# Kernel optimization log

Hardware: AMD Instinct MI355X
Metric: run time of the kernel (lower is better)

## Reference

```python
import jax, jax.numpy as jnp
import numpy as np

T, B, F = 197, 64, 768      # tokens (hardcoded 197 in module), batch, width
N, K = 8, 2                 # num_experts, top-k
CAP = int(197 * 1.0 * K / N)  # capacity = 49
H = 4 * F                   # expert hidden (c_fc out)
G = F // 4                  # gate hidden


def setup_inputs() -> dict:
    key = jax.random.key(0)
    ks = jax.random.split(key, 9)
    s = 0.02
    return {
        "x":   jax.random.normal(ks[0], (T, B, F), jnp.float32),
        # gate: Linear(F, F/4) -> ReLU -> Linear(F/4, N)
        "Wg1": jax.random.normal(ks[1], (F, G), jnp.float32) * s,
        "bg1": jnp.zeros((G,), jnp.float32),
        "Wg2": jax.random.normal(ks[2], (G, N), jnp.float32) * s,
        "bg2": jnp.zeros((N,), jnp.float32),
        # experts: per-expert Linear(F, 4F) -> ReLU -> Linear(4F, F), stacked over N
        "W1":  jax.random.normal(ks[3], (N, F, H), jnp.float32) * s,
        "b1":  jnp.zeros((N, H), jnp.float32),
        "W2":  jax.random.normal(ks[4], (N, H, F), jnp.float32) * s,
        "b2":  jnp.zeros((N, F), jnp.float32),
    }


def reference(x, Wg1, bg1, Wg2, bg2, W1, b1, W2, b2):
    # gating: softmax over experts (dim=2)
    logits = jax.nn.relu(x @ Wg1 + bg1) @ Wg2 + bg2          # [T,B,N]
    gw = jax.nn.softmax(logits, axis=2)                      # [T,B,N]

    # dense all-expert MLP (as-written: every expert on every token)
    h = jax.nn.relu(jnp.einsum('tbf,nfh->tbnh', x, W1) + b1)  # [T,B,N,H]
    eo = jnp.einsum('tbnh,nhf->tbnf', h, W2) + b2             # [T,B,N,F]

    # top-k expert mask (dim=2)
    _, idx = jax.lax.top_k(gw, K)                             # [T,B,K]
    mask_exp = jnp.any(jnp.arange(N)[None, None, None, :] == idx[..., None], axis=2)
    cw = gw * mask_exp                                        # [T,B,N]

    # capacity mask: top-CAP tokens per (batch, expert) along dim 0
    cwT = jnp.moveaxis(cw, 0, -1)                             # [B,N,T]
    _, idx2 = jax.lax.top_k(cwT, CAP)                         # [B,N,CAP]
    mask_cap = jnp.any(jnp.arange(T)[None, None, None, :] == idx2[..., None], axis=2)  # [B,N,T]
    fw = cw * jnp.moveaxis(mask_cap, -1, 0)                   # [T,B,N]

    # combine selected expert outputs, residual-style subtract
    out = jnp.einsum('tbnf,tbn->tbf', eo, fw) - x             # [T,B,F]
    return out
```

## Files before the change

kernel.cpp:

```cpp
#include <hip/hip_runtime.h>
#include <hip/hip_bf16.h>
#include <math.h>
#include <stdint.h>

#define T_ 197
#define B_ 64
#define F_ 768
#define N_ 8
#define CAP_ 49
#define H_ 3072
#define G_ 192
#define TB_ (T_*B_)
#define NBN_ (B_*N_)
#define ME_ 3200
#define MR_ 3136
#define MT_ 25600
#define HCF_ 384
#define NPF_ 8

using bf16x8 = __attribute__((ext_vector_type(8))) short;
using f32x4  = __attribute__((ext_vector_type(4))) float;

__device__ __forceinline__ unsigned short f2bf(float v) {
    __hip_bfloat16 h = __float2bfloat16(v);
    return __builtin_bit_cast(unsigned short, h);
}
__device__ __forceinline__ float bf2f(unsigned short u) {
    unsigned int w = ((unsigned int)u) << 16;
    return __builtin_bit_cast(float, w);
}

#define GLL16(g, l) __builtin_amdgcn_global_load_lds( \
    (const __attribute__((address_space(1))) unsigned int*)(uintptr_t)(g), \
    (__attribute__((address_space(3))) unsigned int*)(uintptr_t)(l), 16, 0, 0)

__device__ __forceinline__ int xcd_swz(int bid, int nblk) {
    int q = nblk >> 3, r = nblk & 7;
    int xcd = bid & 7, idx = bid >> 3;
    int base = (xcd < r) ? xcd * (q + 1) : r * (q + 1) + (xcd - r) * q;
    return base + idx;
}

__global__ void k_init_out(const float* __restrict__ x, float* __restrict__ out) {
    int i = blockIdx.x * blockDim.x + threadIdx.x;
    const float4* xv = (const float4*)x;
    float4* ov = (float4*)out;
    float4 v = xv[i];
    ov[i] = make_float4(-v.x, -v.y, -v.z, -v.w);
}

__global__ __launch_bounds__(256) void k_gate1(
        const float* __restrict__ x, const float* __restrict__ Wg1,
        float* __restrict__ gs_part) {
    __shared__ float xs[2][64 * 32];
    __shared__ float wt[2][64][36];
    int bid = blockIdx.x;
    int bm = bid % 197; int rest = bid / 197;
    int bn = rest % 3, kh = rest / 3;
    int m0 = bm * 64, n0 = bn * 64, k0 = kh * 384;
    int tid = threadIdx.x, lane = tid & 63, wid = tid >> 6;
    int tc = tid & 15, tr = tid >> 4;
    float acc[4][4] = {};
    const float* xbase = x + (size_t)m0 * F_ + k0;
    float wreg[8];

    auto issueX = [&](int buf, int t) {
        int kb = t * 32;
        #pragma unroll
        for (int i = 0; i < 2; ++i) {
            int r0 = wid * 16 + i * 8;
            GLL16(xbase + (size_t)(r0 + (lane >> 3)) * F_ + kb + (lane & 7) * 4,
                  &xs[buf][r0 * 32]);
        }
    };
    auto loadW = [&](int t) {
        int kb = k0 + t * 32;
        #pragma unroll
        for (int i = 0; i < 8; ++i) {
            int idx = tid + i * 256;
            int kk = idx >> 6, nn = idx & 63;
            wreg[i] = Wg1[(size_t)(kb + kk) * G_ + n0 + nn];
        }
    };
    auto writeW = [&](int buf) {
        #pragma unroll
        for (int i = 0; i < 8; ++i) {
            int idx = tid + i * 256;
            int kk = idx >> 6, nn = idx & 63;
            wt[buf][nn][kk] = wreg[i];
        }
    };

    loadW(0); issueX(0, 0); writeW(0);
    __syncthreads();
    int cur = 0;
    for (int t = 0; t < 12; ++t) {
        if (t < 11) { loadW(t + 1); issueX(cur ^ 1, t + 1); }
        const float* xc = &xs[cur][0];
        #pragma unroll
        for (int kq = 0; kq < 8; ++kq) {
            float4 a[4], b[4];
            #pragma unroll
            for (int i = 0; i < 4; ++i) a[i] = *(const float4*)(xc + (tr * 4 + i) * 32 + kq * 4);
            #pragma unroll
            for (int j = 0; j < 4; ++j) b[j] = *(const float4*)&wt[cur][tc + 16 * j][kq * 4];
            #pragma unroll
            for (int i = 0; i < 4; ++i)
                #pragma unroll
                for (int j = 0; j < 4; ++j)
                    acc[i][j] += a[i].x * b[j].x + a[i].y * b[j].y + a[i].z * b[j].z + a[i].w * b[j].w;
        }
        if (t < 11) writeW(cur ^ 1);
        __syncthreads();
        cur ^= 1;
    }
    float* gp = gs_part + (size_t)kh * TB_ * G_;
    #pragma unroll
    for (int j = 0; j < 4; ++j) {
        int c = n0 + tc + 16 * j;
        #pragma unroll
        for (int i = 0; i < 4; ++i) {
            int r = m0 + tr * 4 + i;
            gp[(size_t)r * G_ + c] = acc[i][j];
        }
    }
}

__global__ __launch_bounds__(256) void k_gate2(
        const float* __restrict__ gs_part, const float* __restrict__ bg1,
        const float* __restrict__ Wg2, const float* __restrict__ bg2,
        float* __restrict__ cw, int* __restrict__ ecnt) {
    __shared__ float gsh[32][200];
    __shared__ float wg2s[G_ * N_];
    __shared__ float lg[32][8];
    int tid = threadIdx.x;
    int id0 = blockIdx.x * 32;

    for (int i = tid; i < 32 * 48; i += 256) {
        int r = i / 48, c4 = i % 48;
        const float* p0 = gs_part + (size_t)(id0 + r) * G_ + c4 * 4;
        float4 a = *(const float4*)p0;
        float4 b = *(const float4*)(p0 + (size_t)TB_ * G_);
        float4 g = *(const float4*)(bg1 + c4 * 4);
        float4 v;
        v.x = fmaxf(a.x + b.x + g.x, 0.f);
        v.y = fmaxf(a.y + b.y + g.y, 0.f);
        v.z = fmaxf(a.z + b.z + g.z, 0.f);
        v.w = fmaxf(a.w + b.w + g.w, 0.f);
        ((float4*)&gsh[r][0])[c4] = v;
    }
    for (int i = tid; i < G_ * N_; i += 256) wg2s[i] = Wg2[i];
    __syncthreads();

    int tk = tid >> 3, n = tid & 7;
    float a = bg2[n];
    for (int k = 0; k < G_; ++k) a += gsh[tk][k] * wg2s[k * N_ + n];
    lg[tk][n] = a;
    __syncthreads();

    if (tid < 32) {
        int tk2 = tid;
        float p[8];
        float m = lg[tk2][0];
        #pragma unroll
        for (int nn = 1; nn < 8; ++nn) m = fmaxf(m, lg[tk2][nn]);
        float s = 0.f;
        #pragma unroll
        for (int nn = 0; nn < 8; ++nn) { p[nn] = expf(lg[tk2][nn] - m); s += p[nn]; }
        float inv = 1.f / s;
        #pragma unroll
        for (int nn = 0; nn < 8; ++nn) p[nn] *= inv;
        int i1 = 0; float v1 = p[0];
        #pragma unroll
        for (int nn = 1; nn < 8; ++nn) if (p[nn] > v1) { v1 = p[nn]; i1 = nn; }
        int i2 = -1; float v2 = -1.f;
        #pragma unroll
        for (int nn = 0; nn < 8; ++nn) if (nn != i1 && p[nn] > v2) { v2 = p[nn]; i2 = nn; }
        int id = id0 + tk2;
        int t = id / B_, b = id % B_;
        ecnt[id] = 0;
        #pragma unroll
        for (int nn = 0; nn < 8; ++nn) {
            float v = (nn == i1 || nn == i2) ? p[nn] : 0.f;
            cw[((size_t)(b * N_ + nn)) * T_ + t] = v;
        }
    }
}

__global__ __launch_bounds__(256) void k_gate(
        const float* __restrict__ x, const float* __restrict__ Wg1,
        const float* __restrict__ bg1, const float* __restrict__ Wg2,
        const float* __restrict__ bg2, float* __restrict__ cw,
        int* __restrict__ ecnt) {
    __shared__ float xsh[8][F_];
    __shared__ float gsl[8][G_];
    __shared__ float lg[8][N_];
    int tid = threadIdx.x;
    int id0 = blockIdx.x * 8;

    int gid = blockIdx.x * 256 + tid;
    if (gid < TB_ && ecnt) ecnt[gid] = 0;

    const float4* xv = (const float4*)(x + (size_t)id0 * F_);
    float4* xshv = (float4*)&xsh[0][0];
    for (int idx = tid; idx < 8 * (F_/4); idx += 256) xshv[idx] = xv[idx];
    __syncthreads();

    if (tid < G_) {
        float acc[8];
        float bb = bg1[tid];
        #pragma unroll
        for (int tk = 0; tk < 8; ++tk) acc[tk] = bb;
        for (int k = 0; k < F_; ++k) {
            float w = Wg1[k * G_ + tid];
            #pragma unroll
            for (int tk = 0; tk < 8; ++tk) acc[tk] += xsh[tk][k] * w;
        }
        #pragma unroll
        for (int tk = 0; tk < 8; ++tk) gsl[tk][tid] = fmaxf(acc[tk], 0.f);
    }
    __syncthreads();

    if (tid < 64) {
        int tk = tid >> 3, n = tid & 7;
        float acc = bg2[n];
        for (int k = 0; k < G_; ++k) acc += gsl[tk][k] * Wg2[k * N_ + n];
        lg[tk][n] = acc;
    }
    __syncthreads();

    if (tid < 8) {
        int tk = tid;
        float p[8];
        float m = lg[tk][0];
        #pragma unroll
        for (int n = 1; n < 8; ++n) m = fmaxf(m, lg[tk][n]);
        float s = 0.f;
        #pragma unroll
        for (int n = 0; n < 8; ++n) { p[n] = expf(lg[tk][n] - m); s += p[n]; }
        float inv = 1.f / s;
        #pragma unroll
        for (int n = 0; n < 8; ++n) p[n] *= inv;
        int i1 = 0; float v1 = p[0];
        #pragma unroll
        for (int n = 1; n < 8; ++n) if (p[n] > v1) { v1 = p[n]; i1 = n; }
        int i2 = -1; float v2 = -1.f;
        #pragma unroll
        for (int n = 0; n < 8; ++n) if (n != i1 && p[n] > v2) { v2 = p[n]; i2 = n; }
        int id = id0 + tk;
        int t = id / B_, b = id % B_;
        #pragma unroll
        for (int n = 0; n < 8; ++n) {
            float v = (n == i1 || n == i2) ? p[n] : 0.f;
            cw[((size_t)(b * N_ + n)) * T_ + t] = v;
        }
    }
}

__global__ __launch_bounds__(256) void k_capacity(
        const float* __restrict__ cw, int* __restrict__ toks,
        float* __restrict__ wts, int* __restrict__ counts,
        int* __restrict__ ecnt, int* __restrict__ erow) {
    __shared__ float v[T_];
    __shared__ int keep[T_];
    int tid = threadIdx.x;
    int bn = blockIdx.x;
    int b = bn >> 3, n = bn & 7;
    if (tid < T_) v[tid] = cw[(size_t)bn * T_ + tid];
    __syncthreads();
    int kp = 0; float my = 0.f;
    if (tid < T_) {
        my = v[tid];
        int rank = 0;
        for (int t2 = 0; t2 < T_; ++t2) {
            float vt = v[t2];
            rank += (vt > my) || (vt == my && t2 < tid);
        }
        kp = (rank < CAP_) && (my > 0.f);
    }
    if (tid < T_) keep[tid] = kp;
    __syncthreads();
    if (tid < T_ && kp) {
        int slot = 0;
        for (int t2 = 0; t2 < T_; ++t2) slot += (t2 < tid) ? keep[t2] : 0;
        toks[bn * CAP_ + slot] = tid;
        wts[bn * CAP_ + slot] = my;
        if (ecnt) {
            int orow = tid * B_ + b;
            int pos = atomicAdd(&ecnt[orow], 1);
            erow[orow * 2 + pos] = n * ME_ + b * CAP_ + slot;
        }
    }
    if (tid == 0) {
        int tot = 0;
        for (int t2 = 0; t2 < T_; ++t2) tot += keep[t2];
        counts[bn] = tot;
    }
}

__global__ __launch_bounds__(256) void k_repack(
        const float* __restrict__ W, unsigned short* __restrict__ WT, int K, int J) {
    __shared__ float tile[64][65];
    int bid = blockIdx.x;
    int nk = K >> 6, nj = J >> 6;
    int kt = bid % nk; bid /= nk;
    int jt = bid % nj; int e = bid / nj;
    int k0 = kt * 64, j0 = jt * 64;
    int tid = threadIdx.x;
    int jr = (tid & 15) << 2;
    int kr = tid >> 4;
    const float* src = W + ((size_t)e * K + k0) * J + j0;
    #pragma unroll
    for (int i = 0; i < 4; ++i) {
        float4 v = *(const float4*)(src + (size_t)(kr + 16 * i) * J + jr);
        *(float4*)&tile[kr + 16 * i][jr] = v;
    }
    __syncthreads();
    int c = tid & 7;
    int jrow = tid >> 3;
    #pragma unroll
    for (int i = 0; i < 2; ++i) {
        int j = jrow + 32 * i;
        float f[8];
        #pragma unroll
        for (int s = 0; s < 8; ++s) f[s] = tile[c * 8 + s][j];
        uint4 u;
        u.x = f2bf(f[0]) | ((unsigned)f2bf(f[1]) << 16);
        u.y = f2bf(f[2]) | ((unsigned)f2bf(f[3]) << 16);
        u.z = f2bf(f[4]) | ((unsigned)f2bf(f[5]) << 16);
        u.w = f2bf(f[6]) | ((unsigned)f2bf(f[7]) << 16);
        int jg = j0 + j;
        char* drow = (char*)WT + ((size_t)e * J + jg) * (size_t)K * 2 + (size_t)(k0 >> 6) * 128;
        *(uint4*)(drow + ((c << 4) ^ ((jg & 7) << 4))) = u;
    }
}

__global__ __launch_bounds__(256) void k_gather(
        const float* __restrict__ x, const int* __restrict__ toks,
        const int* __restrict__ counts, unsigned short* __restrict__ Xg) {
    int gi = blockIdx.x * 256 + threadIdx.x;
    int R = gi / 96, c = gi - R * 96;
    int e = R / ME_, re = R - e * ME_;
    uint4 val = make_uint4(0u, 0u, 0u, 0u);
    if (re < MR_) {
        int g = re / CAP_, slot = re - g * CAP_;
        int bn = g * N_ + e;
        if (slot < counts[bn]) {
            int t = toks[bn * CAP_ + slot];
            const float* xp = x + ((size_t)t * B_ + g) * F_ + c * 8;
            float4 v0 = *(const float4*)xp;
            float4 v1 = *(const float4*)(xp + 4);
            val.x = f2bf(v0.x) | ((unsigned)f2bf(v0.y) << 16);
            val.y = f2bf(v0.z) | ((unsigned)f2bf(v0.w) << 16);
            val.z = f2bf(v1.x) | ((unsigned)f2bf(v1.y) << 16);
            val.w = f2bf(v1.z) | ((unsigned)f2bf(v1.w) << 16);
        }
    }
    int w = (c * 16) & 127;
    char* dst = (char*)Xg + (size_t)R * 1536 + (c >> 3) * 128 + (w ^ ((R & 7) << 4));
    *(uint4*)dst = val;
}

__global__ __launch_bounds__(256) void k_gemm1(
        const unsigned short* __restrict__ W1T, const unsigned short* __restrict__ Xg,
        const float* __restrict__ b1, unsigned short* __restrict__ Hg,
        int e0, int nblk) {
    __shared__ char ldsA[2][16384];
    __shared__ char ldsB[2][16384];
    int swzb = xcd_swz(blockIdx.x, nblk);
    int mt = swzb / 24;
    int jt = swzb % 24;
    int em = mt / 25;
    int e = e0 + em;
    int tid = threadIdx.x, lane = tid & 63, wid = tid >> 6;
    int lr8 = lane >> 3, sl = (lane & 7) << 4;
    const char* Ab = (const char*)W1T + ((size_t)e * H_ + (size_t)jt * 128) * (F_ * 2);
    const char* Bb = (const char*)Xg + ((size_t)e * ME_ + (size_t)(mt % 25) * 128) * (F_ * 2);
    f32x4 acc[4][4] = {};
    int swz = (lane & 7) << 4;
    int q16 = (lane >> 4) << 4;

    auto stage = [&](int buf, int it) {
        int kb = it << 7;
        #pragma unroll
        for (int i = 0; i < 4; ++i) {
            int lr = wid * 32 + i * 8 + lr8;
            GLL16(Ab + (size_t)lr * 1536 + kb + sl, ldsA[buf] + (wid * 32 + i * 8) * 128);
            GLL16(Bb + (size_t)lr * 1536 + kb + sl, ldsB[buf] + (wid * 32 + i * 8) * 128);
        }
    };

    stage(0, 0);
    __syncthreads();
    int cur = 0;
    for (int it = 0; it < 12; ++it) {
        if (it < 11) stage(cur ^ 1, it + 1);
        const char* la = ldsA[cur] + ((wid & 1) * 64) * 128;
        const char* lb = ldsB[cur] + ((wid >> 1) * 64) * 128;
        #pragma unroll
        for (int ks = 0; ks < 2; ++ks) {
            bf16x8 af[4], bfr[4];
            int kk = (ks * 64 + q16) ^ swz;
            #pragma unroll
            for (int t = 0; t < 4; ++t) {
                int ro = (16 * t + (lane & 15)) * 128;
                af[t]  = *(const bf16x8*)(la + ro + kk);
                bfr[t] = *(const bf16x8*)(lb + ro + kk);
            }
            #pragma unroll
            for (int ti = 0; ti < 4; ++ti)
                #pragma unroll
                for (int tm = 0; tm < 4; ++tm)
                    acc[ti][tm] = __builtin_amdgcn_mfma_f32_16x16x32_bf16(af[ti], bfr[tm], acc[ti][tm], 0, 0, 0);
        }
        __syncthreads();
        cur ^= 1;
    }
    int jl0 = jt * 128 + (wid & 1) * 64;
    int ml0 = mt * 128 + (wid >> 1) * 64;
    const float* b1p = b1 + (size_t)e * H_;
    #pragma unroll
    for (int tj = 0; tj < 4; ++tj) {
        int jc = jl0 + 16 * tj + ((lane >> 4) << 2);
        float bb0 = b1p[jc], bb1 = b1p[jc + 1], bb2 = b1p[jc + 2], bb3 = b1p[jc + 3];
        #pragma unroll
        for (int tm = 0; tm < 4; ++tm) {
            int m = ml0 + 16 * tm + (lane & 15);
            f32x4 a = acc[tj][tm];
            unsigned int u0 = f2bf(fmaxf(a[0] + bb0, 0.f)) | ((unsigned)f2bf(fmaxf(a[1] + bb1, 0.f)) << 16);
            unsigned int u1 = f2bf(fmaxf(a[2] + bb2, 0.f)) | ((unsigned)f2bf(fmaxf(a[3] + bb3, 0.f)) << 16);
            int w = (jc * 2) & 127;
            char* dst = (char*)Hg + (size_t)m * (H_ * 2) + ((jc * 2) & ~127) + (w ^ ((m & 7) << 4));
            *(uint2*)dst = make_uint2(u0, u1);
        }
    }
}

__global__ __launch_bounds__(256) void k_gemm2(
        const unsigned short* __restrict__ W2T, const unsigned short* __restrict__ Hg,
        const float* __restrict__ b2, const float* __restrict__ wts,
        const int* __restrict__ counts, unsigned short* __restrict__ Og,
        int e0, int nblk) {
    __shared__ char ldsA[2][16384];
    __shared__ char ldsB[2][16384];
    int swzb = xcd_swz(blockIdx.x, nblk);
    int mt = swzb / 6;
    int ft = swzb % 6;
    int em = mt / 25;
    int e = e0 + em;
    int tid = threadIdx.x, lane = tid & 63, wid = tid >> 6;
    int lr8 = lane >> 3, sl = (lane & 7) << 4;
    const char* Ab = (const char*)W2T + ((size_t)e * F_ + (size_t)ft * 128) * (H_ * 2);
    const char* Bb = (const char*)Hg + (size_t)mt * 128 * (H_ * 2);
    f32x4 acc[4][4] = {};
    int swz = (lane & 7) << 4;
    int q16 = (lane >> 4) << 4;

    auto stage = [&](int buf, int it) {
        int kb = it << 7;
        #pragma unroll
        for (int i = 0; i < 4; ++i) {
            int lr = wid * 32 + i * 8 + lr8;
            GLL16(Ab + (size_t)lr * 6144 + kb + sl, ldsA[buf] + (wid * 32 + i * 8) * 128);
            GLL16(Bb + (size_t)lr * 6144 + kb + sl, ldsB[buf] + (wid * 32 + i * 8) * 128);
        }
    };

    stage(0, 0);
    __syncthreads();
    int cur = 0;
    for (int it = 0; it < 48; ++it) {
        if (it < 47) stage(cur ^ 1, it + 1);
        const char* la = ldsA[cur] + ((wid & 1) * 64) * 128;
        const char* lb = ldsB[cur] + ((wid >> 1) * 64) * 128;
        #pragma unroll
        for (int ks = 0; ks < 2; ++ks) {
            bf16x8 af[4], bfr[4];
            int kk = (ks * 64 + q16) ^ swz;
            #pragma unroll
            for (int t = 0; t < 4; ++t) {
                int ro = (16 * t + (lane & 15)) * 128;
                af[t]  = *(const bf16x8*)(la + ro + kk);
                bfr[t] = *(const bf16x8*)(lb + ro + kk);
            }
            #pragma unroll
            for (int ti = 0; ti < 4; ++ti)
                #pragma unroll
                for (int tm = 0; tm < 4; ++tm)
                    acc[ti][tm] = __builtin_amdgcn_mfma_f32_16x16x32_bf16(af[ti], bfr[tm], acc[ti][tm], 0, 0, 0);
        }
        __syncthreads();
        cur ^= 1;
    }
    int fl0 = ft * 128 + (wid & 1) * 64;
    int ml0 = mt * 128 + (wid >> 1) * 64;
    const float* b2p = b2 + (size_t)e * F_;
    float fwv[4]; int mrow[4];
    #pragma unroll
    for (int tm = 0; tm < 4; ++tm) {
        int m = ml0 + 16 * tm + (lane & 15);
        int re = m - em * ME_;
        float fw = 0.f;
        if (re < MR_) {
            int g = re / CAP_;
            int slot = re - g * CAP_;
            int bn = g * N_ + e;
            if (slot < counts[bn]) fw = wts[bn * CAP_ + slot];
        }
        fwv[tm] = fw;
        mrow[tm] = e0 * ME_ + m;
    }
    #pragma unroll
    for (int tf = 0; tf < 4; ++tf) {
        int f = fl0 + 16 * tf + ((lane >> 4) << 2);
        float c0 = b2p[f], c1 = b2p[f + 1], c2 = b2p[f + 2], c3 = b2p[f + 3];
        #pragma unroll
        for (int tm = 0; tm < 4; ++tm) {
            f32x4 a = acc[tf][tm];
            float fw = fwv[tm];
            unsigned int u0 = f2bf(fw * (a[0] + c0)) | ((unsigned)f2bf(fw * (a[1] + c1)) << 16);
            unsigned int u1 = f2bf(fw * (a[2] + c2)) | ((unsigned)f2bf(fw * (a[3] + c3)) << 16);
            *(uint2*)((char*)Og + (size_t)mrow[tm] * (F_ * 2) + f * 2) = make_uint2(u0, u1);
        }
    }
}

__global__ __launch_bounds__(256) void k_combine(
        const float* __restrict__ x, const unsigned short* __restrict__ Og,
        const int* __restrict__ ecnt, const int* __restrict__ erow,
        float* __restrict__ out) {
    int idx = blockIdx.x * 256 + threadIdx.x;
    int row = idx / 192, c4 = idx - row * 192;
    float4 s = make_float4(0.f, 0.f, 0.f, 0.f);
    int c = ecnt[row];
    if (c > 0) {
        ushort4 u = *(const ushort4*)(Og + (size_t)erow[row * 2] * F_ + c4 * 4);
        s.x += bf2f(u.x); s.y += bf2f(u.y); s.z += bf2f(u.z); s.w += bf2f(u.w);
    }
    if (c > 1) {
        ushort4 u = *(const ushort4*)(Og + (size_t)erow[row * 2 + 1] * F_ + c4 * 4);
        s.x += bf2f(u.x); s.y += bf2f(u.y); s.z += bf2f(u.z); s.w += bf2f(u.w);
    }
    float4 xv = ((const float4*)x)[idx];
    ((float4*)out)[idx] = make_float4(s.x - xv.x, s.y - xv.y, s.z - xv.z, s.w - xv.w);
}

__global__ __launch_bounds__(HCF_) void k_fc1(
        const float* __restrict__ x, const float* __restrict__ W1,
        const float* __restrict__ b1, const int* __restrict__ toks,
        const int* __restrict__ counts, __hip_bfloat16* __restrict__ h, int pass) {
    __shared__ float xs[25][F_];
    int tid = threadIdx.x;
    int bn = blockIdx.x >> 1;
    int half = blockIdx.x & 1;
    int r0 = half * 25;
    int b = bn >> 3, n = bn & 7;
    int c = counts[bn];
    for (int idx = tid; idx < 25 * (F_/4); idx += HCF_) {
        int r = idx / (F_/4), k4 = idx % (F_/4);
        int gr = r0 + r;
        float4 val = make_float4(0.f, 0.f, 0.f, 0.f);
        if (gr < c) {
            int t = toks[bn * CAP_ + gr];
            val = ((const float4*)(x + ((size_t)(t * B_ + b)) * F_))[k4];
        }
        ((float4*)&xs[r][0])[k4] = val;
    }
    __syncthreads();
    int j = pass * HCF_ + tid;
    const float* w1p = W1 + (size_t)n * F_ * H_ + j;
    float bias = b1[n * H_ + j];
    float acc[25];
    #pragma unroll
    for (int r = 0; r < 25; ++r) acc[r] = bias;
    const float4* xsv = (const float4*)&xs[0][0];
    for (int k4 = 0; k4 < F_/4; ++k4) {
        float w0 = w1p[(size_t)(4*k4+0) * H_];
        float w1v = w1p[(size_t)(4*k4+1) * H_];
        float w2v = w1p[(size_t)(4*k4+2) * H_];
        float w3v = w1p[(size_t)(4*k4+3) * H_];
        #pragma unroll
        for (int r = 0; r < 25; ++r) {
            float4 xv = xsv[r * (F_/4) + k4];
            acc[r] += xv.x*w0 + xv.y*w1v + xv.z*w2v + xv.w*w3v;
        }
    }
    __hip_bfloat16* hp = h + ((size_t)bn * CAP_ + r0) * HCF_ + tid;
    #pragma unroll
    for (int r = 0; r < 25; ++r) {
        int gr = r0 + r;
        if (gr < CAP_) hp[(size_t)r * HCF_] = __float2bfloat16(fmaxf(acc[r], 0.f));
    }
}

__global__ __launch_bounds__(768) void k_fc2(
        const float* __restrict__ W2, const float* __restrict__ b2,
        const int* __restrict__ toks, const float* __restrict__ wts,
        const int* __restrict__ counts, const __hip_bfloat16* __restrict__ h,
        float* __restrict__ out, int pass) {
    __shared__ float hs[CAP_][HCF_];
    int tid = threadIdx.x;
    int bn = blockIdx.x;
    int c = counts[bn];
    if (c == 0) return;
    int b = bn >> 3, n = bn & 7;
    const ushort4* hv = (const ushort4*)(h + (size_t)bn * CAP_ * HCF_);
    for (int idx = tid; idx < CAP_ * (HCF_/4); idx += 768) {
        ushort4 u = hv[idx];
        float4 fv;
        fv.x = __bfloat162float(*(const __hip_bfloat16*)&u.x);
        fv.y = __bfloat162float(*(const __hip_bfloat16*)&u.y);
        fv.z = __bfloat162float(*(const __hip_bfloat16*)&u.z);
        fv.w = __bfloat162float(*(const __hip_bfloat16*)&u.w);
        ((float4*)&hs[0][0])[idx] = fv;
    }
    __syncthreads();
    int f = tid;
    const float* w2p = W2 + (size_t)n * H_ * F_ + (size_t)(pass * HCF_) * F_ + f;
    float acc[CAP_];
    #pragma unroll
    for (int r = 0; r < CAP_; ++r) acc[r] = 0.f;
    for (int j4 = 0; j4 < HCF_/4; ++j4) {
        float w0 = w2p[(size_t)(4*j4+0) * F_];
        float w1v = w2p[(size_t)(4*j4+1) * F_];
        float w2v = w2p[(size_t)(4*j4+2) * F_];
        float w3v = w2p[(size_t)(4*j4+3) * F_];
        #pragma unroll
        for (int r = 0; r < CAP_; ++r) {
            float4 hh = ((const float4*)&hs[r][0])[j4];
            acc[r] += hh.x*w0 + hh.y*w1v + hh.z*w2v + hh.w*w3v;
        }
    }
    float bias = (pass == 0) ? b2[n * F_ + f] : 0.f;
    #pragma unroll
    for (int r = 0; r < CAP_; ++r) {
        if (r < c) {
            int t = toks[bn * CAP_ + r];
            float fw = wts[bn * CAP_ + r];
            atomicAdd(&out[((size_t)(t * B_ + b)) * F_ + f], fw * (acc[r] + bias));
        }
    }
}

extern "C" void kernel_launch(void* const* d_in, const int* in_sizes, int n_in,
                              void* d_out, int out_size, void* d_ws, size_t ws_size,
                              hipStream_t stream) {
    const float* x   = (const float*)d_in[0];
    const float* Wg1 = (const float*)d_in[1];
    const float* bg1 = (const float*)d_in[2];
    const float* Wg2 = (const float*)d_in[3];
    const float* bg2 = (const float*)d_in[4];
    const float* W1  = (const float*)d_in[5];
    const float* b1  = (const float*)d_in[6];
    const float* W2  = (const float*)d_in[7];
    const float* b2  = (const float*)d_in[8];
    float* out = (float*)d_out;

    size_t oW1T  = 0;
    size_t oW2T  = oW1T + (size_t)N_ * H_ * F_ * 2;
    size_t oXg   = oW2T + (size_t)N_ * H_ * F_ * 2;
    size_t oCw   = oXg  + (size_t)MT_ * F_ * 2;
    size_t oWts  = oCw  + (size_t)NBN_ * T_ * 4;
    size_t oTok  = oWts + (size_t)NBN_ * CAP_ * 4;
    size_t oCnt  = oTok + (size_t)NBN_ * CAP_ * 4;
    size_t oEcnt = oCnt + (size_t)NBN_ * 4;
    size_t oErow = oEcnt + (size_t)TB_ * 4;
    size_t oOg   = oErow + (size_t)TB_ * 8;
    size_t oHg   = oOg  + (size_t)MT_ * F_ * 2;
    size_t hgPerExpert = (size_t)ME_ * H_ * 2;

    int grp = 0;
    if (ws_size >= oHg + 8 * hgPerExpert) grp = 8;
    else if (ws_size >= oHg + 4 * hgPerExpert) grp = 4;
    else if (ws_size >= oHg + 2 * hgPerExpert) grp = 2;

    if (grp > 0) {
        unsigned short* W1T = (unsigned short*)((char*)d_ws + oW1T);
        unsigned short* W2T = (unsigned short*)((char*)d_ws + oW2T);
        unsigned short* Xg  = (unsigned short*)((char*)d_ws + oXg);
        unsigned short* Og  = (unsigned short*)((char*)d_ws + oOg);
        unsigned short* Hg  = (unsigned short*)((char*)d_ws + oHg);
        float* gs_part = (float*)((char*)d_ws + oHg);
        float* cw   = (float*)((char*)d_ws + oCw);
        float* wts  = (float*)((char*)d_ws + oWts);
        int* toks   = (int*)((char*)d_ws + oTok);
        int* counts = (int*)((char*)d_ws + oCnt);
        int* ecnt   = (int*)((char*)d_ws + oEcnt);
        int* erow   = (int*)((char*)d_ws + oErow);

        k_gate1<<<197 * 3 * 2, 256, 0, stream>>>(x, Wg1, gs_part);
        k_gate2<<<TB_ / 32, 256, 0, stream>>>(gs_part, bg1, Wg2, bg2, cw, ecnt);
        k_capacity<<<NBN_, 256, 0, stream>>>(cw, toks, wts, counts, ecnt, erow);
        k_repack<<<N_ * (F_/64) * (H_/64), 256, 0, stream>>>(W1, W1T, F_, H_);
        k_repack<<<N_ * (H_/64) * (F_/64), 256, 0, stream>>>(W2, W2T, H_, F_);
        k_gather<<<(MT_ * 96) / 256, 256, 0, stream>>>(x, toks, counts, Xg);
        for (int e0 = 0; e0 < N_; e0 += grp) {
            int nblk1 = grp * 25 * 24;
            int nblk2 = grp * 25 * 6;
            k_gemm1<<<nblk1, 256, 0, stream>>>(W1T, Xg, b1, Hg, e0, nblk1);
            k_gemm2<<<nblk2, 256, 0, stream>>>(W2T, Hg, b2, wts, counts, Og, e0, nblk2);
        }
        k_combine<<<(TB_ * 192) / 256, 256, 0, stream>>>(x, Og, ecnt, erow, out);
    } else {
        __hip_bfloat16* h = (__hip_bfloat16*)d_ws;
        float* cw  = (float*)((char*)d_ws + (size_t)NBN_ * CAP_ * HCF_ * 2);
        float* wts = cw + (size_t)NBN_ * T_;
        int* toks  = (int*)(wts + NBN_ * CAP_);
        int* counts = toks + NBN_ * CAP_;
        k_init_out<<<(TB_ * F_) / 1024, 256, 0, stream>>>(x, out);
        k_gate<<<TB_ / 8, 256, 0, stream>>>(x, Wg1, bg1, Wg2, bg2, cw, nullptr);
        k_capacity<<<NBN_, 256, 0, stream>>>(cw, toks, wts, counts, nullptr, nullptr);
        for (int p = 0; p < NPF_; ++p) {
            k_fc1<<<NBN_ * 2, HCF_, 0, stream>>>(x, W1, b1, toks, counts, h, p);
            k_fc2<<<NBN_, 768, 0, stream>>>(W2, b2, toks, wts, counts, h, out, p);
        }
    }
}
```

Baseline: 553.0 us.

## Split gate GEMM K dimension four ways and simplify to single-buffered LDS

The gate first-layer GEMM now splits the reduction dimension into four partial sums instead of two, doubling the block count, and gate2 sums four partials. The LDS tiles become single-buffered with register prefetch, replacing the direct global-to-LDS async loads, and use padded rows to reduce bank conflicts. This aims to raise occupancy and parallelism on a small kernel, at the cost of more partial-sum traffic, extra barriers, and a larger workspace footprint for gs_part, which aliases Hg.

```diff
diff --git a/kernel.cpp b/kernel.cpp
--- a/kernel.cpp
+++ b/kernel.cpp
@@ -15,6 +15,7 @@
 #define ME_ 3200
 #define MR_ 3136
 #define MT_ 25600
+#define KH_ 4
 #define HCF_ 384
 #define NPF_ 8
 
@@ -52,67 +53,67 @@
 __global__ __launch_bounds__(256) void k_gate1(
         const float* __restrict__ x, const float* __restrict__ Wg1,
         float* __restrict__ gs_part) {
-    __shared__ float xs[2][64 * 32];
-    __shared__ float wt[2][64][36];
+    __shared__ float xs[64][35];
+    __shared__ float wt[64][35];
     int bid = blockIdx.x;
     int bm = bid % 197; int rest = bid / 197;
     int bn = rest % 3, kh = rest / 3;
-    int m0 = bm * 64, n0 = bn * 64, k0 = kh * 384;
-    int tid = threadIdx.x, lane = tid & 63, wid = tid >> 6;
+    int m0 = bm * 64, n0 = bn * 64, k0 = kh * (F_ / KH_);
+    int tid = threadIdx.x;
     int tc = tid & 15, tr = tid >> 4;
     float acc[4][4] = {};
-    const float* xbase = x + (size_t)m0 * F_ + k0;
-    float wreg[8];
-
-    auto issueX = [&](int buf, int t) {
-        int kb = t * 32;
+
+    int xr0 = tid >> 3, xc4 = (tid & 7) << 2;
+    int wnn = tid & 63, wkw = tid >> 6;
+
+    float4 xreg[2];
+    float4 wreg[2];
+
+    auto loadRegs = [&](int t) {
+        int kb = k0 + t * 32;
         #pragma unroll
         for (int i = 0; i < 2; ++i) {
-            int r0 = wid * 16 + i * 8;
-            GLL16(xbase + (size_t)(r0 + (lane >> 3)) * F_ + kb + (lane & 7) * 4,
-                  &xs[buf][r0 * 32]);
+            int r = xr0 + i * 32;
+            xreg[i] = *(const float4*)(x + (size_t)(m0 + r) * F_ + kb + xc4);
+        }
+        #pragma unroll
+        for (int i = 0; i < 2; ++i) {
+            int kkg = (wkw * 2 + i) * 4;
+            const float* wp = Wg1 + (size_t)(kb + kkg) * G_ + n0 + wnn;
+            wreg[i].x = wp[0];
+            wreg[i].y = wp[G_];
+            wreg[i].z = wp[2 * G_];
+            wreg[i].w = wp[3 * G_];
         }
     };
-    auto loadW = [&](int t) {
-        int kb = k0 + t * 32;
-        #pragma unroll
-        for (int i = 0; i < 8; ++i) {
-            int idx = tid + i * 256;
-            int kk = idx >> 6, nn = idx & 63;
-            wreg[i] = Wg1[(size_t)(kb + kk) * G_ + n0 + nn];
-        }
+    auto writeLDS = [&]() {
+        #pragma unroll
+        for (int i = 0; i < 2; ++i)
+            *(float4*)&xs[xr0 + i * 32][xc4] = xreg[i];
+        #pragma unroll
+        for (int i = 0; i < 2; ++i)
+            *(float4*)&wt[wnn][(wkw * 2 + i) * 4] = wreg[i];
     };
-    auto writeW = [&](int buf) {
-        #pragma unroll
-        for (int i = 0; i < 8; ++i) {
-            int idx = tid + i * 256;
-            int kk = idx >> 6, nn = idx & 63;
-            wt[buf][nn][kk] = wreg[i];
-        }
-    };
-
-    loadW(0); issueX(0, 0); writeW(0);
-    __syncthreads();
-    int cur = 0;
-    for (int t = 0; t < 12; ++t) {
-        if (t < 11) { loadW(t + 1); issueX(cur ^ 1, t + 1); }
-        const float* xc = &xs[cur][0];
+
+    loadRegs(0);
+    for (int t = 0; t < 6; ++t) {
+        __syncthreads();
+        writeLDS();
+        __syncthreads();
+        if (t < 5) loadRegs(t + 1);
         #pragma unroll
         for (int kq = 0; kq < 8; ++kq) {
             float4 a[4], b[4];
             #pragma unroll
-            for (int i = 0; i < 4; ++i) a[i] = *(const float4*)(xc + (tr * 4 + i) * 32 + kq * 4);
+            for (int i = 0; i < 4; ++i) a[i] = *(const float4*)&xs[tr * 4 + i][kq * 4];
             #pragma unroll
-            for (int j = 0; j < 4; ++j) b[j] = *(const float4*)&wt[cur][tc + 16 * j][kq * 4];
+            for (int j = 0; j < 4; ++j) b[j] = *(const float4*)&wt[tc + 16 * j][kq * 4];
             #pragma unroll
             for (int i = 0; i < 4; ++i)
                 #pragma unroll
                 for (int j = 0; j < 4; ++j)
                     acc[i][j] += a[i].x * b[j].x + a[i].y * b[j].y + a[i].z * b[j].z + a[i].w * b[j].w;
         }
-        if (t < 11) writeW(cur ^ 1);
-        __syncthreads();
-        cur ^= 1;
     }
     float* gp = gs_part + (size_t)kh * TB_ * G_;
     #pragma unroll
@@ -141,12 +142,14 @@
         const float* p0 = gs_part + (size_t)(id0 + r) * G_ + c4 * 4;
         float4 a = *(const float4*)p0;
         float4 b = *(const float4*)(p0 + (size_t)TB_ * G_);
+        float4 c = *(const float4*)(p0 + 2 * (size_t)TB_ * G_);
+        float4 d = *(const float4*)(p0 + 3 * (size_t)TB_ * G_);
         float4 g = *(const float4*)(bg1 + c4 * 4);
         float4 v;
-        v.x = fmaxf(a.x + b.x + g.x, 0.f);
-        v.y = fmaxf(a.y + b.y + g.y, 0.f);
-        v.z = fmaxf(a.z + b.z + g.z, 0.f);
-        v.w = fmaxf(a.w + b.w + g.w, 0.f);
+        v.x = fmaxf(a.x + b.x + c.x + d.x + g.x, 0.f);
+        v.y = fmaxf(a.y + b.y + c.y + d.y + g.y, 0.f);
+        v.z = fmaxf(a.z + b.z + c.z + d.z + g.z, 0.f);
+        v.w = fmaxf(a.w + b.w + c.w + d.w + g.w, 0.f);
         ((float4*)&gsh[r][0])[c4] = v;
     }
     for (int i = tid; i < G_ * N_; i += 256) wg2s[i] = Wg2[i];
@@ -688,7 +691,7 @@
         int* ecnt   = (int*)((char*)d_ws + oEcnt);
         int* erow   = (int*)((char*)d_ws + oErow);
 
-        k_gate1<<<197 * 3 * 2, 256, 0, stream>>>(x, Wg1, gs_part);
+        k_gate1<<<197 * 3 * KH_, 256, 0, stream>>>(x, Wg1, gs_part);
         k_gate2<<<TB_ / 32, 256, 0, stream>>>(gs_part, bg1, Wg2, bg2, cw, ecnt);
         k_capacity<<<NBN_, 256, 0, stream>>>(cw, toks, wts, counts, ecnt, erow);
         k_repack<<<N_ * (F_/64) * (H_/64), 256, 0, stream>>>(W1, W1T, F_, H_);
```

New measurement: 513.3 us. 7.2% less time.
